# Optimization experiments

Measured on AMD Instinct MI355X. Metric: run time of the kernel, lower is better.

## Reference

```python
import jax, jax.numpy as jnp
import numpy as np

DEPTH = 12  # perfect binary tree: 2**DEPTH - 1 internal nodes, 2**DEPTH leaf children


def setup_inputs() -> dict:
    key = jax.random.key(0)
    k0, k1, k2, k3, k4 = jax.random.split(key, 5)
    H = 1024   # hidden_size
    I = 1024   # input_size
    N = 2 ** DEPTH - 1  # internal nodes, heap order (root = 0)
    scale = 0.02  # keep gates out of saturation
    emb = jax.random.normal(k0, (N, I), jnp.float32)
    W_ih = jax.random.normal(k1, (8 * H, I), jnp.float32) * scale
    W_hh = jax.random.normal(k2, (8 * H, 2 * H), jnp.float32) * scale
    b_ih = jax.random.normal(k3, (8 * H,), jnp.float32) * scale
    b_hh = jax.random.normal(k4, (8 * H,), jnp.float32) * scale
    return {"emb": emb, "W_ih": W_ih, "W_hh": W_hh, "b_ih": b_ih, "b_hh": b_hh}


def reference(emb, W_ih, W_hh, b_ih, b_hh):
    # Batched-by-level Tree-LSTM over a perfect binary tree in heap order.
    # nn.LSTM hidden size is 2H; node state passed upward is the first H dims.
    H2 = W_hh.shape[1]          # 2 * hidden_size
    H = H2 // 2
    b = b_ih + b_hh
    # Leaves: hidden = cell = zeros((1, H)) per the module's base case.
    h = jnp.zeros((2 ** DEPTH, H), emb.dtype)
    c = jnp.zeros((2 ** DEPTH, H), emb.dtype)
    for k in range(DEPTH - 1, -1, -1):  # bottom-up over levels
        n = 2 ** k
        # cat((a.hidden, b.hidden), dim=1): children of node j are 2j, 2j+1
        h_cat = h.reshape(n, H2)
        c_cat = c.reshape(n, H2)
        x = emb[n - 1: 2 * n - 1]  # level-k embeddings (heap indices n-1 .. 2n-2)
        gates = x @ W_ih.T + h_cat @ W_hh.T + b  # (n, 8H)
        i_, f_, g_, o_ = jnp.split(gates, 4, axis=1)  # PyTorch gate order i,f,g,o
        c_new = jax.nn.sigmoid(f_) * c_cat + jax.nn.sigmoid(i_) * jnp.tanh(g_)
        h_new = jax.nn.sigmoid(o_) * jnp.tanh(c_new)
        h = h_new[:, :H]  # slice back to hidden_size, as the module does
        c = c_new[:, :H]
    # root hidden and cell, each (1, H)
    return jnp.concatenate([h, c], axis=1)
```

## Files before the change

kernel.cpp:

```cpp
#include <hip/hip_runtime.h>
#include <hip/hip_bf16.h>
#include <math.h>


#define TREE_DEPTH 12

typedef unsigned short u16;
typedef unsigned int u32;
typedef __attribute__((ext_vector_type(8))) short bf16x8;
typedef __attribute__((ext_vector_type(4))) float f32x4;
typedef __attribute__((ext_vector_type(8))) unsigned short u16x8;
typedef __attribute__((ext_vector_type(2))) unsigned int u32x2;

__device__ __forceinline__ void gload16(const void* g, void* l) {
    __builtin_amdgcn_global_load_lds(
        (const __attribute__((address_space(1))) u32*)g,
        (__attribute__((address_space(3))) u32*)l, 16, 0, 0);
}

__device__ __forceinline__ u16 f2bf(float f) {
    __hip_bfloat16 h = __float2bfloat16(f);
    return *reinterpret_cast<u16*>(&h);
}
__device__ __forceinline__ u16 f2h(float f) {
    _Float16 h = (_Float16)f;
    return *reinterpret_cast<u16*>(&h);
}
__device__ __forceinline__ float h2f(u16 u) {
    _Float16 h;
    *reinterpret_cast<u16*>(&h) = u;
    return (float)h;
}
__device__ __forceinline__ float fsig(float x) {
    return 1.0f / (1.0f + __expf(-x));
}
__device__ __forceinline__ float ftanh(float x) {
    return 1.0f - 2.0f / (1.0f + __expf(2.0f * x));
}

__global__ void prep(const float* __restrict__ Wih,
                     const float* __restrict__ Whh,
                     const float* __restrict__ emb,
                     const float* __restrict__ b_ih,
                     const float* __restrict__ b_hh,
                     u16* __restrict__ Wih_p, u16* __restrict__ Whh_p,
                     u16* __restrict__ xb, float* __restrict__ bge) {
    const int bid = blockIdx.x;
    if (bid < 12288) {
        const int b = bid & 4095;
        const int seg = bid >> 12;
        const int x = b & 7, t = b >> 3;
        const int e = ((t & 3) * 8 + x) * 128 + (t >> 2);
        const int g = (e >> 4) & 3;
        const int j = (e >> 6) * 16 + (e & 15);
        const int wr = g * 2048 + j;
        const int col = threadIdx.x * 4;
        f32x4 v;
        u16* dst;
        if (seg == 0) {
            v = __builtin_nontemporal_load(
                (const f32x4*)(Wih + (size_t)wr * 1024 + col));
            dst = Wih_p + (size_t)e * 1024 + col;
        } else {
            v = __builtin_nontemporal_load(
                (const f32x4*)(Whh + (size_t)wr * 2048 + (seg - 1) * 1024 + col));
            dst = Whh_p + (size_t)e * 2048 + (seg - 1) * 1024 + col;
        }
        u32x2 p;
        p[0] = (u32)f2bf(v[0]) | ((u32)f2bf(v[1]) << 16);
        p[1] = (u32)f2bf(v[2]) | ((u32)f2bf(v[3]) << 16);
        *reinterpret_cast<u32x2*>(dst) = p;
    } else if (bid < 16383) {
        size_t idx = ((size_t)(bid - 12288) * 256 + threadIdx.x) * 4;
        f32x4 v = __builtin_nontemporal_load((const f32x4*)(emb + idx));
        u32x2 p;
        p[0] = (u32)f2bf(v[0]) | ((u32)f2bf(v[1]) << 16);
        p[1] = (u32)f2bf(v[2]) | ((u32)f2bf(v[3]) << 16);
        *reinterpret_cast<u32x2*>(xb + idx) = p;
    } else {
        int e = (bid - 16383) * 256 + threadIdx.x;
        int g = (e >> 4) & 3;
        int j = (e >> 6) * 16 + (e & 15);
        int r = g * 2048 + j;
        bge[e] = b_ih[r] + b_hh[r];
    }
}

__global__ __launch_bounds__(256) void gemm_gx(
    const u16* __restrict__ xb, const u16* __restrict__ Wp,
    const float* __restrict__ bge, u16* __restrict__ GX,
    u16* __restrict__ hdst, float* __restrict__ cdst)
{
    __shared__ u16 smem[128 * 140];

    const int gx_ = gridDim.x;
    int b = blockIdx.x + gx_ * blockIdx.y;
    const int x = b & 7, t = b >> 3;
    const int ct = (t & 3) * 8 + x;
    const int mt = t >> 2;
    const int m0 = mt * 128, c0 = ct * 128;

    const int tid = threadIdx.x, lane = tid & 63, w = tid >> 6;
    const int wr = (w >> 1) * 64, wc = (w & 1) * 64;

    f32x4 acc[4][4];
    #pragma unroll
    for (int i = 0; i < 4; ++i)
        #pragma unroll
        for (int j = 0; j < 4; ++j)
            acc[i][j] = f32x4{0.f, 0.f, 0.f, 0.f};

    const u16* gp[8];
    u16* dl[8];
    #pragma unroll
    for (int i = 0; i < 8; ++i) {
        const int s = tid + i * 256;
        const int r = s >> 3;
        const int o = (s & 7) * 16;
        const int ke = (o ^ ((r & 7) << 4)) >> 1;
        gp[i] = (r < 128) ? xb + (size_t)(m0 + r) * 1024 + ke
                          : Wp + (size_t)(c0 + r - 128) * 1024 + ke;
        dl[i] = smem + s * 8;
    }

    const int fl = lane & 15;
    const int kunit = (lane >> 4) * 16;

    for (int k0 = 0; k0 < 1024; k0 += 64) {
        #pragma unroll
        for (int i = 0; i < 8; ++i) { gload16(gp[i], dl[i]); gp[i] += 64; }
        __syncthreads();
        #pragma unroll
        for (int ks = 0; ks < 2; ++ks) {
            bf16x8 a_[4], b_[4];
            #pragma unroll
            for (int i = 0; i < 4; ++i) {
                const int ar = wr + i * 16 + fl;
                const int byo = (ks * 64 + kunit) ^ ((ar & 7) << 4);
                a_[i] = *reinterpret_cast<const bf16x8*>(
                    reinterpret_cast<const char*>(smem + ar * 64) + byo);
            }
            #pragma unroll
            for (int j = 0; j < 4; ++j) {
                const int br = 128 + wc + j * 16 + fl;
                const int byo = (ks * 64 + kunit) ^ ((br & 7) << 4);
                b_[j] = *reinterpret_cast<const bf16x8*>(
                    reinterpret_cast<const char*>(smem + br * 64) + byo);
            }
            #pragma unroll
            for (int i = 0; i < 4; ++i)
                #pragma unroll
                for (int j = 0; j < 4; ++j)
                    acc[i][j] = __builtin_amdgcn_mfma_f32_16x16x32_bf16(
                        a_[i], b_[j], acc[i][j], 0, 0, 0);
        }
        __syncthreads();
    }

    const int rg = (lane >> 4) * 4;
    if (m0 < 2047) {
        #pragma unroll
        for (int i = 0; i < 4; ++i)
            #pragma unroll
            for (int j = 0; j < 4; ++j) {
                const float bv = bge[c0 + wc + j * 16 + fl];
                #pragma unroll
                for (int r = 0; r < 4; ++r)
                    smem[(wr + i * 16 + rg + r) * 140 + (wc + j * 16 + fl)] =
                        f2h(acc[i][j][r] + bv);
            }
        __syncthreads();
        const int row_ = tid >> 4, chunk = tid & 15;
        #pragma unroll
        for (int it = 0; it < 8; ++it) {
            const int row = it * 16 + row_;
            if (m0 + row < 2047) {
                u16x8 v = *reinterpret_cast<const u16x8*>(
                    &smem[row * 140 + chunk * 8]);
                __builtin_nontemporal_store(
                    v, (u16x8*)(GX + (size_t)(m0 + row) * 4096 + c0 + chunk * 8));
            }
        }
    }
    if (m0 + 127 >= 2047) {
        const int jj = ((c0 + wc) >> 6) * 16 + fl;
        const float bi  = bge[c0 + wc + fl];
        const float bgg = bge[c0 + wc + 32 + fl];
        const float bo  = bge[c0 + wc + 48 + fl];
        #pragma unroll
        for (int i = 0; i < 4; ++i) {
            #pragma unroll
            for (int r = 0; r < 4; ++r) {
                const int m = m0 + wr + i * 16 + rg + r;
                if (m < 2047 || m >= 4095) continue;
                const int mm = m - 2047;
                const float cn = fsig(acc[i][0][r] + bi) * ftanh(acc[i][2][r] + bgg);
                const float hn = fsig(acc[i][3][r] + bo) * ftanh(cn);
                hdst[(size_t)(mm >> 1) * 2048 + (mm & 1) * 1024 + jj] = f2bf(hn);
                if (!(mm & 1))
                    cdst[(size_t)(mm >> 1) * 1024 + jj] = cn;
            }
        }
    }
}

template <int MI, int MW, int NW, int KG, int KSX>
__global__ __launch_bounds__(MW* NW* KG * 64) void fused_level(
    const u16* __restrict__ A, const u16* __restrict__ Wp,
    const u16* __restrict__ GXl, const float* __restrict__ cprev,
    u16* __restrict__ hnext, float* __restrict__ cnext,
    float* __restrict__ outp, int n, float* __restrict__ pout)
{
    constexpr int BM = MI * 16 * MW;
    constexpr int BN = NW * 64;
    constexpr int S = MW * NW;
    constexpr int NFR = MI * 4;
    constexpr int RC = NFR > 8 ? 8 : NFR;
    constexpr int NP = NFR / RC;
    constexpr int ROWS = BM + BN;
    constexpr int SLOTS = ROWS * 8;
    constexpr int GT = S * 64;
    constexpr int NL = SLOTS / GT;
    static_assert(SLOTS % GT == 0, "slot mapping must be exact");
    constexpr int STG = KG * ROWS * 128;
    constexpr int REDB = (KG > 1) ? (KG - 1) * S * RC * 64 * 16 : 0;
    constexpr int SMEM = STG > REDB ? STG : REDB;
    __shared__ __align__(16) char smem[SMEM];

    const int gx_ = gridDim.x;
    int b = blockIdx.x + gx_ * blockIdx.y;
    const int x = b & 7;
    int t = b >> 3;
    int ct, mt;
    if constexpr (NW == 2) {
        ct = (t & 3) * 8 + x; mt = t >> 2;
    } else {
        const int lo = t & 1; t >>= 1;
        ct = ((t & 3) * 8 + x) * 2 + lo; mt = t >> 2;
    }
    const int m0 = mt * BM;
    const int c0 = ct * BN;

    const int tid = threadIdx.x;
    const int lane = tid & 63;
    const int w = tid >> 6;
    const int kg = w / S;
    const int slot = w % S;
    const int wm = slot / NW;
    const int wn = slot % NW;

    const int Kc = (2048 / KSX) / KG;
    const int kbeg = (int)blockIdx.z * (2048 / KSX) + kg * Kc;

    u16* buf = (u16*)smem + (size_t)kg * ROWS * 64;

    const int gtid = slot * 64 + lane;
    const u16* gp[NL];
    u16* dl[NL];
    #pragma unroll
    for (int i = 0; i < NL; ++i) {
        const int s = gtid + i * GT;
        const int r = s >> 3;
        const int o = (s & 7) * 16;
        const int ke = (o ^ ((r & 7) << 4)) >> 1;
        if (r < BM) {
            int ar = m0 + r;
            if (ar >= n) ar = n - 1;
            gp[i] = A + (size_t)ar * 2048 + kbeg + ke;
        } else {
            gp[i] = Wp + (size_t)(c0 + r - BM) * 2048 + kbeg + ke;
        }
        dl[i] = buf + s * 8;
    }

    f32x4 acc[MI][4];
    #pragma unroll
    for (int mi = 0; mi < MI; ++mi)
        #pragma unroll
        for (int f = 0; f < 4; ++f)
            acc[mi][f] = f32x4{0.f, 0.f, 0.f, 0.f};

    const int fl = lane & 15;
    const int kunit = (lane >> 4) * 16;
    const int ar0 = wm * MI * 16;
    const int bc0 = BM;

    for (int k0 = 0; k0 < Kc; k0 += 64) {
        #pragma unroll
        for (int i = 0; i < NL; ++i) { gload16(gp[i], dl[i]); gp[i] += 64; }
        __syncthreads();
        #pragma unroll
        for (int ks = 0; ks < 2; ++ks) {
            bf16x8 a_[MI], b_[4];
            #pragma unroll
            for (int mi = 0; mi < MI; ++mi) {
                const int ar = ar0 + mi * 16 + fl;
                const int byo = (ks * 64 + kunit) ^ ((ar & 7) << 4);
                a_[mi] = *reinterpret_cast<const bf16x8*>(
                    reinterpret_cast<const char*>(buf + ar * 64) + byo);
            }
            #pragma unroll
            for (int f = 0; f < 4; ++f) {
                const int br = bc0 + wn * 64 + f * 16 + fl;
                const int byo = (ks * 64 + kunit) ^ ((br & 7) << 4);
                b_[f] = *reinterpret_cast<const bf16x8*>(
                    reinterpret_cast<const char*>(buf + br * 64) + byo);
            }
            #pragma unroll
            for (int mi = 0; mi < MI; ++mi)
                #pragma unroll
                for (int f = 0; f < 4; ++f)
                    acc[mi][f] = __builtin_amdgcn_mfma_f32_16x16x32_bf16(
                        a_[mi], b_[f], acc[mi][f], 0, 0, 0);
        }
        __syncthreads();
    }

    if constexpr (KG > 1) {
        f32x4* red = reinterpret_cast<f32x4*>(smem);
        #pragma unroll
        for (int pass = 0; pass < NP; ++pass) {
            if (kg > 0) {
                #pragma unroll
                for (int f = 0; f < RC; ++f) {
                    const int fr = pass * RC + f;
                    red[(((kg - 1) * S + slot) * RC + f) * 64 + lane] =
                        acc[fr >> 2][fr & 3];
                }
            }
            __syncthreads();
            if (kg == 0) {
                #pragma unroll
                for (int q = 1; q < KG; ++q)
                    #pragma unroll
                    for (int f = 0; f < RC; ++f) {
                        const int fr = pass * RC + f;
                        f32x4 v = red[(((q - 1) * S + slot) * RC + f) * 64 + lane];
                        acc[fr >> 2][fr & 3][0] += v[0];
                        acc[fr >> 2][fr & 3][1] += v[1];
                        acc[fr >> 2][fr & 3][2] += v[2];
                        acc[fr >> 2][fr & 3][3] += v[3];
                    }
            }
            __syncthreads();
        }
    }

    if (kg != 0) return;

    if constexpr (KSX > 1) {
        float* po = pout + (size_t)blockIdx.z * n * 4096;
        #pragma unroll
        for (int mi = 0; mi < MI; ++mi)
            #pragma unroll
            for (int f = 0; f < 4; ++f)
                #pragma unroll
                for (int r = 0; r < 4; ++r) {
                    const int m = m0 + wm * MI * 16 + mi * 16 + (lane >> 4) * 4 + r;
                    if (m < n)
                        po[(size_t)m * 4096 + c0 + wn * 64 + f * 16 + fl] =
                            acc[mi][f][r];
                }
        return;
    }

    const int j = ((c0 + wn * 64) >> 6) * 16 + fl;
    #pragma unroll
    for (int mi = 0; mi < MI; ++mi) {
        #pragma unroll
        for (int r = 0; r < 4; ++r) {
            const int m = m0 + wm * MI * 16 + mi * 16 + (lane >> 4) * 4 + r;
            if (m >= n) continue;
            const u16* gx = GXl + (size_t)m * 4096 + c0 + wn * 64 + fl;
            const float i_ = acc[mi][0][r] + h2f(__builtin_nontemporal_load(gx));
            const float f_ = acc[mi][1][r] + h2f(__builtin_nontemporal_load(gx + 16));
            const float g_ = acc[mi][2][r] + h2f(__builtin_nontemporal_load(gx + 32));
            const float o_ = acc[mi][3][r] + h2f(__builtin_nontemporal_load(gx + 48));
            const float cc = __builtin_nontemporal_load(cprev + (size_t)m * 1024 + j);
            const float cn = fsig(f_) * cc + fsig(i_) * ftanh(g_);
            const float hn = fsig(o_) * ftanh(cn);
            if (hnext)
                hnext[(size_t)(m >> 1) * 2048 + (m & 1) * 1024 + j] = f2bf(hn);
            if (!(m & 1))
                __builtin_nontemporal_store(cn, cnext + (size_t)(m >> 1) * 1024 + j);
            if (outp) { outp[j] = hn; outp[1024 + j] = cn; }
        }
    }
}

__global__ void act_tail(const float* __restrict__ parts, int ksn, size_t stride,
                         const u16* __restrict__ GXl,
                         const float* __restrict__ cprev,
                         u16* __restrict__ hnext, float* __restrict__ cnext,
                         float* __restrict__ outp, int n)
{
    int idx = blockIdx.x * 256 + threadIdx.x;
    if (idx >= n * 256) return;
    const int m = idx >> 8;
    const int j4 = (idx & 255) * 4;
    const int eb = (j4 >> 4) * 64 + (j4 & 15);

    const u16* gx = GXl + (size_t)m * 4096;
    float iv[4], fv[4], gv[4], ov[4];
    #pragma unroll
    for (int t = 0; t < 4; ++t) {
        iv[t] = h2f(gx[eb + t]);
        fv[t] = h2f(gx[eb + 16 + t]);
        gv[t] = h2f(gx[eb + 32 + t]);
        ov[t] = h2f(gx[eb + 48 + t]);
    }
    for (int s = 0; s < ksn; ++s) {
        const float* p = parts + (size_t)s * stride + (size_t)m * 4096;
        #pragma unroll
        for (int t = 0; t < 4; ++t) {
            iv[t] += p[eb + t];
            fv[t] += p[eb + 16 + t];
            gv[t] += p[eb + 32 + t];
            ov[t] += p[eb + 48 + t];
        }
    }
    #pragma unroll
    for (int t = 0; t < 4; ++t) {
        const float cc = cprev[(size_t)m * 1024 + j4 + t];
        const float cn = fsig(fv[t]) * cc + fsig(iv[t]) * ftanh(gv[t]);
        const float hn = fsig(ov[t]) * ftanh(cn);
        if (hnext)
            hnext[(size_t)(m >> 1) * 2048 + (m & 1) * 1024 + j4 + t] = f2bf(hn);
        if (!(m & 1))
            cnext[(size_t)(m >> 1) * 1024 + j4 + t] = cn;
        if (outp) { outp[j4 + t] = hn; outp[1024 + j4 + t] = cn; }
    }
}

extern "C" void kernel_launch(void* const* d_in, const int* in_sizes, int n_in,
                              void* d_out, int out_size, void* d_ws, size_t ws_size,
                              hipStream_t stream) {
    const float* emb  = (const float*)d_in[0];
    const float* W_ih = (const float*)d_in[1];
    const float* W_hh = (const float*)d_in[2];
    const float* b_ih = (const float*)d_in[3];
    const float* b_hh = (const float*)d_in[4];
    float* out = (float*)d_out;

    char* p = (char*)d_ws;
    float* bge  = (float*)p;  p += 16384;
    u16* Wih_p  = (u16*)p;    p += (size_t)4096 * 1024 * 2;
    u16* Whh_p  = (u16*)p;    p += (size_t)4096 * 2048 * 2;
    u16* xb     = (u16*)p;    p += (size_t)4096 * 1024 * 2;
    u16* GX     = (u16*)p;    p += (size_t)4096 * 4096 * 2;
    u16* Hcat   = (u16*)p;    p += (size_t)4096 * 2048 * 2;
    float* cbA  = (float*)p;  p += (size_t)1024 * 1024 * 4;
    float* cbB  = (float*)p;  p += (size_t)1024 * 1024 * 4;
    float* parts = (float*)p; p += (size_t)4 * 32 * 4096 * 4;

    prep<<<16399, 256, 0, stream>>>(W_ih, W_hh, emb, b_ih, b_hh,
                                    Wih_p, Whh_p, xb, bge);

    #define OFF(k) (4096 - (2 << (k)))

    gemm_gx<<<dim3(32, 32), 256, 0, stream>>>(
        xb, Wih_p, bge, GX, Hcat + (size_t)OFF(10) * 2048, cbA);

    const float* cprev = cbA;
    float* cbufs[2] = {cbB, cbA};
    int t = 0;
    for (int k = TREE_DEPTH - 2; k >= 0; --k) {
        const int n = 1 << k;
        const u16* A = Hcat + (size_t)OFF(k) * 2048;
        const u16* GXl = GX + (size_t)(n - 1) * 4096;
        u16* hnext = (k > 0) ? (Hcat + (size_t)OFF(k - 1) * 2048) : nullptr;
        float* cnext = cbufs[t];
        float* outp = (k == 0) ? out : nullptr;

        if (k == 10) {
            fused_level<4, 1, 2, 2, 1><<<dim3(16, 32), 256, 0, stream>>>(
                A, Whh_p, GXl, cprev, hnext, cnext, outp, n, nullptr);
        } else if (k == 9) {
            fused_level<2, 1, 2, 2, 1><<<dim3(16, 32), 256, 0, stream>>>(
                A, Whh_p, GXl, cprev, hnext, cnext, outp, n, nullptr);
        } else if (k == 8) {
            fused_level<1, 1, 1, 4, 1><<<dim3(16, 64), 256, 0, stream>>>(
                A, Whh_p, GXl, cprev, hnext, cnext, outp, n, nullptr);
        } else if (k >= 6) {
            const int gxd = n / 16;
            fused_level<1, 1, 1, 8, 1><<<dim3(gxd, 64), 512, 0, stream>>>(
                A, Whh_p, GXl, cprev, hnext, cnext, outp, n, nullptr);
        } else if (k == 5) {
            fused_level<1, 1, 1, 8, 2><<<dim3(2, 64, 2), 512, 0, stream>>>(
                A, Whh_p, nullptr, nullptr, nullptr, nullptr, nullptr, n, parts);
            act_tail<<<n, 256, 0, stream>>>(parts, 2, (size_t)n * 4096,
                                            GXl, cprev, hnext, cnext, outp, n);
        } else {
            const int gxd = (n >= 16) ? n / 16 : 1;
            fused_level<1, 1, 1, 8, 4><<<dim3(gxd, 64, 4), 512, 0, stream>>>(
                A, Whh_p, nullptr, nullptr, nullptr, nullptr, nullptr, n, parts);
            act_tail<<<n, 256, 0, stream>>>(parts, 4, (size_t)n * 4096,
                                            GXl, cprev, hnext, cnext, outp, n);
        }
        cprev = cnext; t ^= 1;
    }
}
```

Before: 221.5 us.

## Enlarge gemm_gx tiles to 256x256 with double-buffered LDS prefetch

Reworks the input-projection GEMM to use 1024-thread blocks computing 256x256 tiles, with two LDS buffers so the global-to-LDS loads for the next K slice overlap the MFMA work on the current one. Waits use explicit vmcnt counts and raw barriers. The epilogue stages output through LDS in four 64-row chunks because the larger tile no longer fits in one pass. This targets global-load latency and per-tile reload traffic, at the cost of 128KB of LDS per block (one block per CU) and only 256 blocks in the grid.

```diff
diff --git a/kernel.cpp b/kernel.cpp
--- a/kernel.cpp
+++ b/kernel.cpp
@@ -16,6 +16,16 @@
     __builtin_amdgcn_global_load_lds(
         (const __attribute__((address_space(1))) u32*)g,
         (__attribute__((address_space(3))) u32*)l, 16, 0, 0);
+}
+
+template <int N>
+__device__ __forceinline__ void vmwait() {
+    asm volatile("s_waitcnt vmcnt(%0)" :: "n"(N) : "memory");
+}
+__device__ __forceinline__ void rbar() {
+    __builtin_amdgcn_sched_barrier(0);
+    __builtin_amdgcn_s_barrier();
+    __builtin_amdgcn_sched_barrier(0);
 }
 
 __device__ __forceinline__ u16 f2bf(float f) {
@@ -86,22 +96,21 @@
     }
 }
 
-__global__ __launch_bounds__(256) void gemm_gx(
+__global__ __launch_bounds__(1024) void gemm_gx(
     const u16* __restrict__ xb, const u16* __restrict__ Wp,
     const float* __restrict__ bge, u16* __restrict__ GX,
     u16* __restrict__ hdst, float* __restrict__ cdst)
 {
-    __shared__ u16 smem[128 * 140];
-
-    const int gx_ = gridDim.x;
-    int b = blockIdx.x + gx_ * blockIdx.y;
+    __shared__ u16 smem[65536];
+
+    int b = blockIdx.x + 16 * blockIdx.y;
     const int x = b & 7, t = b >> 3;
-    const int ct = (t & 3) * 8 + x;
-    const int mt = t >> 2;
-    const int m0 = mt * 128, c0 = ct * 128;
+    const int ct = (t & 1) * 8 + x;
+    const int mt = t >> 1;
+    const int m0 = mt * 256, c0 = ct * 256;
 
     const int tid = threadIdx.x, lane = tid & 63, w = tid >> 6;
-    const int wr = (w >> 1) * 64, wc = (w & 1) * 64;
+    const int wm = w >> 2, wn = w & 3;
 
     f32x4 acc[4][4];
     #pragma unroll
@@ -110,88 +119,117 @@
         for (int j = 0; j < 4; ++j)
             acc[i][j] = f32x4{0.f, 0.f, 0.f, 0.f};
 
-    const u16* gp[8];
-    u16* dl[8];
-    #pragma unroll
-    for (int i = 0; i < 8; ++i) {
-        const int s = tid + i * 256;
+    u16* bufs[2] = {smem, smem + 32768};
+    const u16* gp[4];
+    u16* dl0[4];
+    u16* dl1[4];
+    #pragma unroll
+    for (int i = 0; i < 4; ++i) {
+        const int s = tid + i * 1024;
         const int r = s >> 3;
         const int o = (s & 7) * 16;
         const int ke = (o ^ ((r & 7) << 4)) >> 1;
-        gp[i] = (r < 128) ? xb + (size_t)(m0 + r) * 1024 + ke
-                          : Wp + (size_t)(c0 + r - 128) * 1024 + ke;
-        dl[i] = smem + s * 8;
+        gp[i] = (r < 256) ? xb + (size_t)(m0 + r) * 1024 + ke
+                          : Wp + (size_t)(c0 + r - 256) * 1024 + ke;
+        dl0[i] = bufs[0] + s * 8;
+        dl1[i] = bufs[1] + s * 8;
     }
 
     const int fl = lane & 15;
     const int kunit = (lane >> 4) * 16;
 
-    for (int k0 = 0; k0 < 1024; k0 += 64) {
-        #pragma unroll
-        for (int i = 0; i < 8; ++i) { gload16(gp[i], dl[i]); gp[i] += 64; }
-        __syncthreads();
-        #pragma unroll
-        for (int ks = 0; ks < 2; ++ks) {
-            bf16x8 a_[4], b_[4];
-            #pragma unroll
-            for (int i = 0; i < 4; ++i) {
-                const int ar = wr + i * 16 + fl;
-                const int byo = (ks * 64 + kunit) ^ ((ar & 7) << 4);
-                a_[i] = *reinterpret_cast<const bf16x8*>(
-                    reinterpret_cast<const char*>(smem + ar * 64) + byo);
-            }
-            #pragma unroll
-            for (int j = 0; j < 4; ++j) {
-                const int br = 128 + wc + j * 16 + fl;
-                const int byo = (ks * 64 + kunit) ^ ((br & 7) << 4);
-                b_[j] = *reinterpret_cast<const bf16x8*>(
-                    reinterpret_cast<const char*>(smem + br * 64) + byo);
-            }
-            #pragma unroll
-            for (int i = 0; i < 4; ++i)
-                #pragma unroll
-                for (int j = 0; j < 4; ++j)
-                    acc[i][j] = __builtin_amdgcn_mfma_f32_16x16x32_bf16(
-                        a_[i], b_[j], acc[i][j], 0, 0, 0);
-        }
-        __syncthreads();
-    }
+    #define STAGE0() { _Pragma("unroll") \
+        for (int i = 0; i < 4; ++i) { gload16(gp[i], dl0[i]); gp[i] += 64; } }
+    #define STAGE1() { _Pragma("unroll") \
+        for (int i = 0; i < 4; ++i) { gload16(gp[i], dl1[i]); gp[i] += 64; } }
+
+    #define COMPUTE(BUF) {                                                   \
+        _Pragma("unroll")                                                    \
+        for (int ks = 0; ks < 2; ++ks) {                                     \
+            bf16x8 a_[4], b_[4];                                             \
+            _Pragma("unroll")                                                \
+            for (int i = 0; i < 4; ++i) {                                    \
+                const int ar = wm * 64 + i * 16 + fl;                        \
+                const int byo = (ks * 64 + kunit) ^ ((ar & 7) << 4);         \
+                a_[i] = *reinterpret_cast<const bf16x8*>(                    \
+                    reinterpret_cast<const char*>((BUF) + ar * 64) + byo);   \
+            }                                                                \
+            _Pragma("unroll")                                                \
+            for (int j = 0; j < 4; ++j) {                                    \
+                const int br = 256 + wn * 64 + j * 16 + fl;                  \
+                const int byo = (ks * 64 + kunit) ^ ((br & 7) << 4);         \
+                b_[j] = *reinterpret_cast<const bf16x8*>(                    \
+                    reinterpret_cast<const char*>((BUF) + br * 64) + byo);   \
+            }                                                                \
+            _Pragma("unroll")                                                \
+            for (int i = 0; i < 4; ++i)                                      \
+                _Pragma("unroll")                                            \
+                for (int j = 0; j < 4; ++j)                                  \
+                    acc[i][j] = __builtin_amdgcn_mfma_f32_16x16x32_bf16(     \
+                        a_[i], b_[j], acc[i][j], 0, 0, 0);                   \
+        } }
+
+    STAGE0();
+    #pragma unroll 2
+    for (int it = 0; it < 16; ++it) {
+        const int cur = it & 1;
+        if (it < 15) {
+            if (cur == 0) STAGE1() else STAGE0();
+            vmwait<4>();
+        } else {
+            vmwait<0>();
+        }
+        rbar();
+        if (cur == 0) COMPUTE(bufs[0]) else COMPUTE(bufs[1]);
+        rbar();
+    }
+    #undef STAGE0
+    #undef STAGE1
+    #undef COMPUTE
 
     const int rg = (lane >> 4) * 4;
     if (m0 < 2047) {
         #pragma unroll
-        for (int i = 0; i < 4; ++i)
+        for (int ch = 0; ch < 4; ++ch) {
+            __syncthreads();
+            if (wm == ch) {
+                #pragma unroll
+                for (int i = 0; i < 4; ++i)
+                    #pragma unroll
+                    for (int j = 0; j < 4; ++j) {
+                        const int col = wn * 64 + j * 16 + fl;
+                        const float bv = bge[c0 + col];
+                        #pragma unroll
+                        for (int r = 0; r < 4; ++r)
+                            smem[(i * 16 + rg + r) * 264 + col] =
+                                f2h(acc[i][j][r] + bv);
+                    }
+            }
+            __syncthreads();
             #pragma unroll
-            for (int j = 0; j < 4; ++j) {
-                const float bv = bge[c0 + wc + j * 16 + fl];
-                #pragma unroll
-                for (int r = 0; r < 4; ++r)
-                    smem[(wr + i * 16 + rg + r) * 140 + (wc + j * 16 + fl)] =
-                        f2h(acc[i][j][r] + bv);
-            }
-        __syncthreads();
-        const int row_ = tid >> 4, chunk = tid & 15;
-        #pragma unroll
-        for (int it = 0; it < 8; ++it) {
-            const int row = it * 16 + row_;
-            if (m0 + row < 2047) {
-                u16x8 v = *reinterpret_cast<const u16x8*>(
-                    &smem[row * 140 + chunk * 8]);
-                __builtin_nontemporal_store(
-                    v, (u16x8*)(GX + (size_t)(m0 + row) * 4096 + c0 + chunk * 8));
-            }
-        }
-    }
-    if (m0 + 127 >= 2047) {
-        const int jj = ((c0 + wc) >> 6) * 16 + fl;
-        const float bi  = bge[c0 + wc + fl];
-        const float bgg = bge[c0 + wc + 32 + fl];
-        const float bo  = bge[c0 + wc + 48 + fl];
+            for (int ps = 0; ps < 2; ++ps) {
+                const int row = ps * 32 + (tid >> 5);
+                const int u8o = (tid & 31) * 8;
+                const int gm = m0 + ch * 64 + row;
+                if (gm < 2047) {
+                    u16x8 v = *reinterpret_cast<const u16x8*>(
+                        &smem[row * 264 + u8o]);
+                    __builtin_nontemporal_store(
+                        v, (u16x8*)(GX + (size_t)gm * 4096 + c0 + u8o));
+                }
+            }
+        }
+    }
+    if (m0 + 255 >= 2047) {
+        const int jj = ((c0 + wn * 64) >> 6) * 16 + fl;
+        const float bi  = bge[c0 + wn * 64 + fl];
+        const float bgg = bge[c0 + wn * 64 + 32 + fl];
+        const float bo  = bge[c0 + wn * 64 + 48 + fl];
         #pragma unroll
         for (int i = 0; i < 4; ++i) {
             #pragma unroll
             for (int r = 0; r < 4; ++r) {
-                const int m = m0 + wr + i * 16 + rg + r;
+                const int m = m0 + wm * 64 + i * 16 + rg + r;
                 if (m < 2047 || m >= 4095) continue;
                 const int mm = m - 2047;
                 const float cn = fsig(acc[i][0][r] + bi) * ftanh(acc[i][2][r] + bgg);
@@ -458,7 +496,7 @@
 
     #define OFF(k) (4096 - (2 << (k)))
 
-    gemm_gx<<<dim3(32, 32), 256, 0, stream>>>(
+    gemm_gx<<<dim3(16, 16), 1024, 0, stream>>>(
         xb, Wih_p, bge, GX, Hcat + (size_t)OFF(10) * 2048, cbA);
 
     const float* cprev = cbA;
```

Result: no change. 222.7 us (+0.5%).
